# Kernel tuning notes

Hardware: AMD Instinct MI355X
Metric: run time of the kernel (lower is better)

Reference implementation:

```python
import jax, jax.numpy as jnp
import numpy as np

RADII = np.array([0.5, 1.0, 1.5, 2.0], dtype=np.float32)
SIGMA = 0.5          # gaussian radial-function width (= radius spacing)
EPS = 1e-8
N_SH = 9             # real spherical harmonics up to l=2
N_BASIS = len(RADII) * N_SH


def real_sh_l2(u):
    """Real spherical harmonics l=0,1,2 of unit vectors u[..., 3] -> [..., 9]."""
    x, y, z = u[..., 0], u[..., 1], u[..., 2]
    one = jnp.ones_like(x)
    return jnp.stack([
        0.28209479 * one,
        0.48860251 * x, 0.48860251 * y, 0.48860251 * z,
        1.09254843 * x * y,
        1.09254843 * y * z,
        0.31539157 * (3.0 * z * z - 1.0),
        1.09254843 * x * z,
        0.54627421 * (x * x - y * y),
    ], axis=-1)


def setup_inputs() -> dict:
    key = jax.random.key(0)
    k1, k2, k3, k4, k5 = jax.random.split(key, 5)
    n, c_in, d_out, b, a = 4, 32, 32, 8192, 32
    inp = jax.random.normal(k1, (n, c_in, b), jnp.float32)
    coords = jax.random.uniform(k2, (n, b, 3), jnp.float32) * 4.0
    neighbors = jax.random.randint(k3, (n, b, a), 0, b)
    relative_mask = jax.random.uniform(k4, (n, b, a), jnp.float32)
    W = jax.random.normal(k5, (d_out, c_in, N_BASIS), jnp.float32) / np.sqrt(c_in * N_BASIS)
    return {"input": inp, "coords": coords, "relative_mask": relative_mask,
            "W": W, "neighbors": neighbors}


def reference(input, coords, relative_mask, W, neighbors):
    n, c, b = input.shape
    idx_n = jnp.arange(n)[:, None, None]                     # [n,1,1]
    # neighbor difference matrix: coords[neighbors] - coords  -> [n,b,a,3]
    neigh_xyz = coords[idx_n, neighbors]
    diff = neigh_xyz - coords[:, :, None, :]
    r = jnp.linalg.norm(diff, axis=-1)                       # [n,b,a]
    u = diff / (r[..., None] + EPS)
    Y = real_sh_l2(u)                                        # [n,b,a,9]
    radii = jnp.asarray(RADII)
    rb = jnp.exp(-((r[..., None] - radii) / SIGMA) ** 2)     # [n,b,a,4]
    basis = (rb[..., :, None] * Y[..., None, :]).reshape(r.shape + (-1,))  # [n,b,a,36]
    # neighbor feature matrix: input[n, :, neighbors[n,b,a]] -> [n,b,a,c]
    feat = input[idx_n, :, neighbors]
    # relative_mask multiplies k over (n,b,a) == masking gathered features
    feat = feat * relative_mask[..., None]
    # fused form of: k[d,c,n,b,a] = sum_k basis[n,b,a,k] W[d,c,k];
    # out[n,d,b] = sum_{c,a} feat[n,b,a,c] * k[d,c,n,b,a]
    M = jnp.einsum('nbac,nbak->nbck', feat, basis)           # [n,b,c,36]
    return jnp.einsum('nbck,dck->ndb', M, W)
```

## Files before the change

### kernel.cpp

```cpp
#include <hip/hip_runtime.h>
#include <hip/hip_bf16.h>


typedef _Float16 f16x8 __attribute__((ext_vector_type(8)));
typedef _Float16 f16x4 __attribute__((ext_vector_type(4)));
typedef __fp16   h16x2 __attribute__((ext_vector_type(2)));
typedef float    f32x4 __attribute__((ext_vector_type(4)));
typedef unsigned int u32;

__device__ __forceinline__ u32 pk16(float a, float b) {
    union { h16x2 v; u32 u; } cv;
    cv.v = __builtin_amdgcn_cvt_pkrtz(a, b);
    return cv.u;
}
__device__ __forceinline__ unsigned short f16bits(float v) {
    const _Float16 hv = (_Float16)v;
    return __builtin_bit_cast(unsigned short, hv);
}

#define BAS_STRIDE 44

__device__ __forceinline__ void geom(float dx, float dy, float dz, float msk, int h_,
                                     float Y[9], float& rbA, float& rbB) {
    const float d2  = dx * dx + dy * dy + dz * dz;
    const float inv = rsqrtf(d2 + 1e-16f);
    const float r   = d2 * inv;
    const float x = dx * inv, y = dy * inv, z = dz * inv;
    Y[0] = 0.28209479f;
    Y[1] = 0.48860251f * x;
    Y[2] = 0.48860251f * y;
    Y[3] = 0.48860251f * z;
    Y[4] = 1.09254843f * x * y;
    Y[5] = 1.09254843f * y * z;
    Y[6] = 0.31539157f * (3.0f * z * z - 1.0f);
    Y[7] = 1.09254843f * x * z;
    Y[8] = 0.54627421f * (x * x - y * y);
    const float sA = r - (h_ ? 1.5f : 0.5f);
    const float sB = r - (h_ ? 2.0f : 1.0f);
    rbA = __expf(sA * sA * -4.0f) * msk;
    rbB = __expf(sB * sB * -4.0f) * msk;
}

__global__ __launch_bounds__(256) void prep_kernel(
    const float* __restrict__ inp, const float* __restrict__ W,
    const float* __restrict__ coords,
    unsigned short* __restrict__ inp_t16, unsigned short* __restrict__ Wfrag,
    float* __restrict__ coords4)
{
    if (blockIdx.x < 1024) {
        __shared__ float T[32][33];
        const int n  = blockIdx.x >> 8;
        const int b0 = (blockIdx.x & 255) << 5;
        const int bx = threadIdx.x & 31;
        const int cy = threadIdx.x >> 5;
        #pragma unroll
        for (int r = 0; r < 4; ++r) {
            const int cc = cy + r * 8;
            T[bx][cc] = inp[((n << 5) + cc) * 8192 + b0 + bx];
        }
        __syncthreads();
        const int cpos = ((bx & 15) << 1) | (bx >> 4);
        #pragma unroll
        for (int r = 0; r < 4; ++r) {
            const int by = cy + r * 8;
            inp_t16[((n << 13) + b0 + by) * 32 + cpos] = f16bits(T[by][bx]);
        }
    } else if (blockIdx.x < 1168) {
        const int t = (blockIdx.x - 1024) * 256 + threadIdx.x;
        if (t < 36 * 2 * 64 * 8) {
            const int j  = t & 7;
            const int l  = (t >> 3) & 63;
            const int dt = (t >> 9) & 1;
            const int kt = t >> 10;
            const int d  = dt * 16 + (l & 15);
            const int c  = ((l >> 4) << 3) + j;
            Wfrag[t] = f16bits(W[d * 1152 + c * 36 + kt]);
        }
    } else {
        const int t = (blockIdx.x - 1168) * 256 + threadIdx.x;
        f32x4 v;
        v[0] = coords[3 * t + 0];
        v[1] = coords[3 * t + 1];
        v[2] = coords[3 * t + 2];
        v[3] = 0.0f;
        *(f32x4*)(coords4 + ((size_t)t << 2)) = v;
    }
}

__global__ __launch_bounds__(512, 4) void se3_main(
    const unsigned short* __restrict__ inp_t16, const float* __restrict__ coords4,
    const float* __restrict__ rmask, const int* __restrict__ neigh,
    const unsigned short* __restrict__ Wfrag, float* __restrict__ out)
{
    __shared__ __align__(16) unsigned short Mb_s[36 * 580];
    __shared__ __align__(16) unsigned short bas[8][37 * BAS_STRIDE];
    __shared__ unsigned short idxs[16][32];
    __shared__ __align__(16) float Cp[8 * 64 * 4];

    const int tid  = threadIdx.x;
    const int lane = tid & 63;
    const int w    = tid >> 6;
    const int l15  = lane & 15;
    const int q    = lane >> 4;
    const int a_   = lane & 31;
    const int h_   = lane >> 5;

    const int blk = blockIdx.x;
    const int n_  = (blk & 7) >> 1;
    const int pos = ((blk >> 3) << 1) | (blk & 1);
    const int b0  = pos << 4;
    const int gp0 = (n_ << 13) | b0;
    const int nbase_pt = n_ << 13;
    const unsigned short* __restrict__ inp_n = inp_t16 + ((size_t)n_ << 18);

    unsigned short* basw = &bas[w][0];

    const int dt  = w >> 2;
    const int seg = w & 3;
    const int kt0 = seg * 9;
    f16x8 wf0, wf1, wf2, wf3, wf4, wf5, wf6, wf7, wf8;
    {
        const unsigned short* wb = &Wfrag[((size_t)((kt0 * 2 + dt) * 64 + lane)) << 3];
        wf0 = *(const f16x8*)(wb + 0 * 1024);
        wf1 = *(const f16x8*)(wb + 1 * 1024);
        wf2 = *(const f16x8*)(wb + 2 * 1024);
        wf3 = *(const f16x8*)(wb + 3 * 1024);
        wf4 = *(const f16x8*)(wb + 4 * 1024);
        wf5 = *(const f16x8*)(wb + 5 * 1024);
        wf6 = *(const f16x8*)(wb + 6 * 1024);
        wf7 = *(const f16x8*)(wb + 7 * 1024);
        wf8 = *(const f16x8*)(wb + 8 * 1024);
    }

    const int ph0 = 2 * l15;
    const int ph1 = (l15 < 2) ? (32 + 2 * l15) : (2 * l15 - 3);
    const int ph2 = (l15 < 4) ? (29 + 2 * l15) : 36;
    const int offB0 = ph0 * BAS_STRIDE + (q << 3);
    const int offB1 = ph1 * BAS_STRIDE + (q << 3);
    const int offB2 = ph2 * BAS_STRIDE + (q << 3);

    const int pA = w << 1, pB = pA | 1;
    const int gpA = gp0 + pA, gpB = gp0 + pB;

    const int   idxA = neigh[(gpA << 5) | a_];
    const int   idxB = neigh[(gpB << 5) | a_];
    const float mskA = rmask[(gpA << 5) | a_];
    const float mskB = rmask[(gpB << 5) | a_];
    const f32x4 cA4 = *(const f32x4*)(coords4 + ((size_t)gpA << 2));
    const f32x4 cB4 = *(const f32x4*)(coords4 + ((size_t)gpB << 2));
    if (lane < 32) {
        idxs[pA][a_] = (unsigned short)idxA;
        idxs[pB][a_] = (unsigned short)idxB;
    }
    const f32x4 nA4 = *(const f32x4*)(coords4 + ((size_t)(nbase_pt + idxA) << 2));
    const f32x4 nB4 = *(const f32x4*)(coords4 + ((size_t)(nbase_pt + idxB) << 2));
    const float dxA = nA4[0] - cA4[0], dyA = nA4[1] - cA4[1], dzA = nA4[2] - cA4[2];
    const float dxB = nB4[0] - cB4[0], dyB = nB4[1] - cB4[1], dzB = nB4[2] - cB4[2];

    u32 gA[8], gB[8];
    #pragma unroll
    for (int j = 0; j < 8; ++j) {
        const int ri = idxs[pA][(q << 3) + j];
        gA[j] = *(const u32*)(inp_n + (((unsigned)ri) << 5) + (l15 << 1));
    }
    #pragma unroll
    for (int j = 0; j < 8; ++j) {
        const int ri = idxs[pB][(q << 3) + j];
        gB[j] = *(const u32*)(inp_n + (((unsigned)ri) << 5) + (l15 << 1));
    }

    float YA[9], YB[9], rbA_A, rbB_A, rbA_B, rbB_B;
    geom(dxA, dyA, dzA, mskA, h_, YA, rbA_A, rbB_A);
    geom(dxB, dyB, dzB, mskB, h_, YB, rbA_B, rbB_B);

    #pragma unroll
    for (int t = 0; t < 18; ++t) {
        const float v = (t < 9) ? rbA_A * YA[t] : rbB_A * YA[t - 9];
        basw[(2 * t + h_) * BAS_STRIDE + a_] = f16bits(v);
    }

    f16x4 blo, bhi;
    blo = *(const f16x4*)&basw[offB0]; bhi = *(const f16x4*)&basw[offB0 + 4];
    const f16x8 BfA0 = __builtin_shufflevector(blo, bhi, 0, 1, 2, 3, 4, 5, 6, 7);
    blo = *(const f16x4*)&basw[offB1]; bhi = *(const f16x4*)&basw[offB1 + 4];
    const f16x8 BfA1 = __builtin_shufflevector(blo, bhi, 0, 1, 2, 3, 4, 5, 6, 7);
    blo = *(const f16x4*)&basw[offB2]; bhi = *(const f16x4*)&basw[offB2 + 4];
    const f16x8 BfA2 = __builtin_shufflevector(blo, bhi, 0, 1, 2, 3, 4, 5, 6, 7);

    union { f16x8 v; u32 u[4]; } afA0, afA1, afB0, afB1;
    #pragma unroll
    for (int j4 = 0; j4 < 4; ++j4) {
        afA0.u[j4] = __builtin_amdgcn_perm(gA[2 * j4 + 1], gA[2 * j4], 0x05040100u);
        afA1.u[j4] = __builtin_amdgcn_perm(gA[2 * j4 + 1], gA[2 * j4], 0x07060302u);
    }
    const f32x4 z4 = {0.0f, 0.0f, 0.0f, 0.0f};
    f32x4 DA00 = __builtin_amdgcn_mfma_f32_16x16x32_f16(afA0.v, BfA0, z4, 0, 0, 0);
    f32x4 DA01 = __builtin_amdgcn_mfma_f32_16x16x32_f16(afA0.v, BfA1, z4, 0, 0, 0);
    f32x4 DA02 = __builtin_amdgcn_mfma_f32_16x16x32_f16(afA0.v, BfA2, z4, 0, 0, 0);
    f32x4 DA10 = __builtin_amdgcn_mfma_f32_16x16x32_f16(afA1.v, BfA0, z4, 0, 0, 0);
    f32x4 DA11 = __builtin_amdgcn_mfma_f32_16x16x32_f16(afA1.v, BfA1, z4, 0, 0, 0);
    f32x4 DA12 = __builtin_amdgcn_mfma_f32_16x16x32_f16(afA1.v, BfA2, z4, 0, 0, 0);

    #pragma unroll
    for (int t = 0; t < 18; ++t) {
        const float v = (t < 9) ? rbA_B * YB[t] : rbB_B * YB[t - 9];
        basw[(2 * t + h_) * BAS_STRIDE + a_] = f16bits(v);
    }
    blo = *(const f16x4*)&basw[offB0]; bhi = *(const f16x4*)&basw[offB0 + 4];
    const f16x8 BfB0 = __builtin_shufflevector(blo, bhi, 0, 1, 2, 3, 4, 5, 6, 7);
    blo = *(const f16x4*)&basw[offB1]; bhi = *(const f16x4*)&basw[offB1 + 4];
    const f16x8 BfB1 = __builtin_shufflevector(blo, bhi, 0, 1, 2, 3, 4, 5, 6, 7);
    blo = *(const f16x4*)&basw[offB2]; bhi = *(const f16x4*)&basw[offB2 + 4];
    const f16x8 BfB2 = __builtin_shufflevector(blo, bhi, 0, 1, 2, 3, 4, 5, 6, 7);

    #pragma unroll
    for (int j4 = 0; j4 < 4; ++j4) {
        afB0.u[j4] = __builtin_amdgcn_perm(gB[2 * j4 + 1], gB[2 * j4], 0x05040100u);
        afB1.u[j4] = __builtin_amdgcn_perm(gB[2 * j4 + 1], gB[2 * j4], 0x07060302u);
    }
    f32x4 DB00 = __builtin_amdgcn_mfma_f32_16x16x32_f16(afB0.v, BfB0, z4, 0, 0, 0);
    f32x4 DB01 = __builtin_amdgcn_mfma_f32_16x16x32_f16(afB0.v, BfB1, z4, 0, 0, 0);
    f32x4 DB02 = __builtin_amdgcn_mfma_f32_16x16x32_f16(afB0.v, BfB2, z4, 0, 0, 0);
    f32x4 DB10 = __builtin_amdgcn_mfma_f32_16x16x32_f16(afB1.v, BfB0, z4, 0, 0, 0);
    f32x4 DB11 = __builtin_amdgcn_mfma_f32_16x16x32_f16(afB1.v, BfB1, z4, 0, 0, 0);
    f32x4 DB12 = __builtin_amdgcn_mfma_f32_16x16x32_f16(afB1.v, BfB2, z4, 0, 0, 0);

    {
        const int rowpA = pA * 36 + (q << 2);
        const int a0 = l15 * 580 + rowpA;
        const int a1 = (16 + l15) * 580 + rowpA;
        *(u32*)&Mb_s[a0]      = pk16(DA00[0], DA00[1]);
        *(u32*)&Mb_s[a0 + 2]  = pk16(DA00[2], DA00[3]);
        *(u32*)&Mb_s[a0 + 16] = pk16(DA10[0], DA10[1]);
        *(u32*)&Mb_s[a0 + 18] = pk16(DA10[2], DA10[3]);
        *(u32*)&Mb_s[a1]      = pk16(DA01[0], DA01[1]);
        *(u32*)&Mb_s[a1 + 2]  = pk16(DA01[2], DA01[3]);
        *(u32*)&Mb_s[a1 + 16] = pk16(DA11[0], DA11[1]);
        *(u32*)&Mb_s[a1 + 18] = pk16(DA11[2], DA11[3]);
        const int rowpB = pB * 36 + (q << 2);
        const int c0 = l15 * 580 + rowpB;
        const int c1 = (16 + l15) * 580 + rowpB;
        *(u32*)&Mb_s[c0]      = pk16(DB00[0], DB00[1]);
        *(u32*)&Mb_s[c0 + 2]  = pk16(DB00[2], DB00[3]);
        *(u32*)&Mb_s[c0 + 16] = pk16(DB10[0], DB10[1]);
        *(u32*)&Mb_s[c0 + 18] = pk16(DB10[2], DB10[3]);
        *(u32*)&Mb_s[c1]      = pk16(DB01[0], DB01[1]);
        *(u32*)&Mb_s[c1 + 2]  = pk16(DB01[2], DB01[3]);
        *(u32*)&Mb_s[c1 + 16] = pk16(DB11[0], DB11[1]);
        *(u32*)&Mb_s[c1 + 18] = pk16(DB11[2], DB11[3]);
        if (l15 < 4) {
            const int a2 = (32 + l15) * 580 + rowpA;
            *(u32*)&Mb_s[a2]      = pk16(DA02[0], DA02[1]);
            *(u32*)&Mb_s[a2 + 2]  = pk16(DA02[2], DA02[3]);
            *(u32*)&Mb_s[a2 + 16] = pk16(DA12[0], DA12[1]);
            *(u32*)&Mb_s[a2 + 18] = pk16(DA12[2], DA12[3]);
            const int c2 = (32 + l15) * 580 + rowpB;
            *(u32*)&Mb_s[c2]      = pk16(DB02[0], DB02[1]);
            *(u32*)&Mb_s[c2 + 2]  = pk16(DB02[2], DB02[3]);
            *(u32*)&Mb_s[c2 + 16] = pk16(DB12[0], DB12[1]);
            *(u32*)&Mb_s[c2 + 18] = pk16(DB12[2], DB12[3]);
        }
    }
    __syncthreads();

    {
        f32x4 acc2 = {0.0f, 0.0f, 0.0f, 0.0f};
        #define P2_STEP(I, WF)                                                       \
        {                                                                            \
            const int mbase = (kt0 + I) * 580 + l15 * 36 + (q << 3);                 \
            const f16x4 mlo = *(const f16x4*)&Mb_s[mbase];                           \
            const f16x4 mhi = *(const f16x4*)&Mb_s[mbase + 4];                       \
            const f16x8 bf  = __builtin_shufflevector(mlo, mhi, 0,1,2,3,4,5,6,7);    \
            acc2 = __builtin_amdgcn_mfma_f32_16x16x32_f16(WF, bf, acc2, 0, 0, 0);    \
        }
        P2_STEP(0, wf0) P2_STEP(1, wf1) P2_STEP(2, wf2)
        P2_STEP(3, wf3) P2_STEP(4, wf4) P2_STEP(5, wf5)
        P2_STEP(6, wf6) P2_STEP(7, wf7) P2_STEP(8, wf8)
        #undef P2_STEP
        *(f32x4*)&Cp[(w * 64 + lane) * 4] = acc2;
    }
    __syncthreads();

    if (w < 2) {
        const int dt2 = w;
        f32x4 s = *(const f32x4*)&Cp[((dt2 * 4 + 0) * 64 + lane) * 4];
        #pragma unroll
        for (int rphase = 1; rphase < 4; ++rphase) {
            const f32x4 t = *(const f32x4*)&Cp[((dt2 * 4 + rphase) * 64 + lane) * 4];
            s[0] += t[0]; s[1] += t[1]; s[2] += t[2]; s[3] += t[3];
        }
        const int drow = dt2 * 16 + (lane >> 4) * 4;
        const int col  = b0 + (lane & 15);
        #pragma unroll
        for (int rr = 0; rr < 4; ++rr) {
            out[(((n_ << 5) + drow + rr) << 13) + col] = s[rr];
        }
    }
}

extern "C" void kernel_launch(void* const* d_in, const int* in_sizes, int n_in,
                              void* d_out, int out_size, void* d_ws, size_t ws_size,
                              hipStream_t stream)
{
    const float* inp    = (const float*)d_in[0];
    const float* coords = (const float*)d_in[1];
    const float* rmask  = (const float*)d_in[2];
    const float* W      = (const float*)d_in[3];
    const int*   neigh  = (const int*)d_in[4];
    float*       outp   = (float*)d_out;

    unsigned short* inp_t16 = (unsigned short*)d_ws;
    unsigned short* Wfrag   = (unsigned short*)((char*)d_ws + (2u << 20));
    float*          coords4 = (float*)((char*)d_ws + (4u << 20));

    prep_kernel<<<1296, 256, 0, stream>>>(inp, W, coords, inp_t16, Wfrag, coords4);
    se3_main<<<2048, 512, 0, stream>>>(inp_t16, coords4, rmask, neigh, Wfrag, outp);
}
```

Before: 88.69 us.

## Make main kernel persistent over four tiles with prefetched neighbor gathers

Each block now handles four 16-point tiles in a loop, so the grid shrinks from 2048 to 512 blocks. The W fragment register loads are amortised across tiles. The next tile's indices, masks, coords and feature gathers are issued before the phase-2 MFMAs of the current tile so their latency overlaps compute. Neighbor indices are shared through ds_bpermute instead of a shared-memory index array, which removes that LDS buffer and its dependency. In exchange, register pressure from the double-buffered gathers goes up, and fewer blocks may leave CUs underfilled.

```diff
diff --git a/kernel.cpp b/kernel.cpp
--- a/kernel.cpp
+++ b/kernel.cpp
@@ -41,6 +41,21 @@
     rbB = __expf(sB * sB * -4.0f) * msk;
 }
 
+__device__ __forceinline__ void gather16(const unsigned short* __restrict__ inp_n,
+                                         int q, int l15, int idxA, int idxB,
+                                         u32* gA, u32* gB) {
+    #pragma unroll
+    for (int j = 0; j < 8; ++j) {
+        const int riA = __builtin_amdgcn_ds_bpermute((((q << 3) + j) << 2), idxA);
+        gA[j] = *(const u32*)(inp_n + (((unsigned)riA) << 5) + (l15 << 1));
+    }
+    #pragma unroll
+    for (int j = 0; j < 8; ++j) {
+        const int riB = __builtin_amdgcn_ds_bpermute((((q << 3) + j) << 2), idxB);
+        gB[j] = *(const u32*)(inp_n + (((unsigned)riB) << 5) + (l15 << 1));
+    }
+}
+
 __global__ __launch_bounds__(256) void prep_kernel(
     const float* __restrict__ inp, const float* __restrict__ W,
     const float* __restrict__ coords,
@@ -94,7 +109,6 @@
 {
     __shared__ __align__(16) unsigned short Mb_s[36 * 580];
     __shared__ __align__(16) unsigned short bas[8][37 * BAS_STRIDE];
-    __shared__ unsigned short idxs[16][32];
     __shared__ __align__(16) float Cp[8 * 64 * 4];
 
     const int tid  = threadIdx.x;
@@ -108,8 +122,6 @@
     const int blk = blockIdx.x;
     const int n_  = (blk & 7) >> 1;
     const int pos = ((blk >> 3) << 1) | (blk & 1);
-    const int b0  = pos << 4;
-    const int gp0 = (n_ << 13) | b0;
     const int nbase_pt = n_ << 13;
     const unsigned short* __restrict__ inp_n = inp_t16 + ((size_t)n_ << 18);
 
@@ -140,162 +152,180 @@
     const int offB2 = ph2 * BAS_STRIDE + (q << 3);
 
     const int pA = w << 1, pB = pA | 1;
-    const int gpA = gp0 + pA, gpB = gp0 + pB;
-
-    const int   idxA = neigh[(gpA << 5) | a_];
-    const int   idxB = neigh[(gpB << 5) | a_];
-    const float mskA = rmask[(gpA << 5) | a_];
-    const float mskB = rmask[(gpB << 5) | a_];
-    const f32x4 cA4 = *(const f32x4*)(coords4 + ((size_t)gpA << 2));
-    const f32x4 cB4 = *(const f32x4*)(coords4 + ((size_t)gpB << 2));
-    if (lane < 32) {
-        idxs[pA][a_] = (unsigned short)idxA;
-        idxs[pB][a_] = (unsigned short)idxB;
-    }
-    const f32x4 nA4 = *(const f32x4*)(coords4 + ((size_t)(nbase_pt + idxA) << 2));
-    const f32x4 nB4 = *(const f32x4*)(coords4 + ((size_t)(nbase_pt + idxB) << 2));
-    const float dxA = nA4[0] - cA4[0], dyA = nA4[1] - cA4[1], dzA = nA4[2] - cA4[2];
-    const float dxB = nB4[0] - cB4[0], dyB = nB4[1] - cB4[1], dzB = nB4[2] - cB4[2];
-
+
+#define LOADTILE(T, oidxA, oidxB, omskA, omskB, ocA, ocB, onA, onB) do {      \
+        const int _gpA = (n_ << 13) + (((pos << 2) | (T)) << 4) + pA;         \
+        const int _gpB = _gpA + 1;                                            \
+        oidxA = neigh[(_gpA << 5) | a_];                                      \
+        oidxB = neigh[(_gpB << 5) | a_];                                      \
+        omskA = rmask[(_gpA << 5) | a_];                                      \
+        omskB = rmask[(_gpB << 5) | a_];                                      \
+        ocA = *(const f32x4*)(coords4 + ((size_t)_gpA << 2));                 \
+        ocB = *(const f32x4*)(coords4 + ((size_t)_gpB << 2));                 \
+        onA = *(const f32x4*)(coords4 + ((size_t)(nbase_pt + oidxA) << 2));   \
+        onB = *(const f32x4*)(coords4 + ((size_t)(nbase_pt + oidxB) << 2));   \
+    } while (0)
+
+    int   idxA, idxB;
+    float mskA, mskB;
+    f32x4 cA4, cB4, nA4, nB4;
+    LOADTILE(0, idxA, idxB, mskA, mskB, cA4, cB4, nA4, nB4);
     u32 gA[8], gB[8];
+    gather16(inp_n, q, l15, idxA, idxB, gA, gB);
+
+    const f32x4 z4 = {0.0f, 0.0f, 0.0f, 0.0f};
+
     #pragma unroll
-    for (int j = 0; j < 8; ++j) {
-        const int ri = idxs[pA][(q << 3) + j];
-        gA[j] = *(const u32*)(inp_n + (((unsigned)ri) << 5) + (l15 << 1));
-    }
-    #pragma unroll
-    for (int j = 0; j < 8; ++j) {
-        const int ri = idxs[pB][(q << 3) + j];
-        gB[j] = *(const u32*)(inp_n + (((unsigned)ri) << 5) + (l15 << 1));
-    }
-
-    float YA[9], YB[9], rbA_A, rbB_A, rbA_B, rbB_B;
-    geom(dxA, dyA, dzA, mskA, h_, YA, rbA_A, rbB_A);
-    geom(dxB, dyB, dzB, mskB, h_, YB, rbA_B, rbB_B);
-
-    #pragma unroll
-    for (int t = 0; t < 18; ++t) {
-        const float v = (t < 9) ? rbA_A * YA[t] : rbB_A * YA[t - 9];
-        basw[(2 * t + h_) * BAS_STRIDE + a_] = f16bits(v);
-    }
-
-    f16x4 blo, bhi;
-    blo = *(const f16x4*)&basw[offB0]; bhi = *(const f16x4*)&basw[offB0 + 4];
-    const f16x8 BfA0 = __builtin_shufflevector(blo, bhi, 0, 1, 2, 3, 4, 5, 6, 7);
-    blo = *(const f16x4*)&basw[offB1]; bhi = *(const f16x4*)&basw[offB1 + 4];
-    const f16x8 BfA1 = __builtin_shufflevector(blo, bhi, 0, 1, 2, 3, 4, 5, 6, 7);
-    blo = *(const f16x4*)&basw[offB2]; bhi = *(const f16x4*)&basw[offB2 + 4];
-    const f16x8 BfA2 = __builtin_shufflevector(blo, bhi, 0, 1, 2, 3, 4, 5, 6, 7);
-
-    union { f16x8 v; u32 u[4]; } afA0, afA1, afB0, afB1;
-    #pragma unroll
-    for (int j4 = 0; j4 < 4; ++j4) {
-        afA0.u[j4] = __builtin_amdgcn_perm(gA[2 * j4 + 1], gA[2 * j4], 0x05040100u);
-        afA1.u[j4] = __builtin_amdgcn_perm(gA[2 * j4 + 1], gA[2 * j4], 0x07060302u);
-    }
-    const f32x4 z4 = {0.0f, 0.0f, 0.0f, 0.0f};
-    f32x4 DA00 = __builtin_amdgcn_mfma_f32_16x16x32_f16(afA0.v, BfA0, z4, 0, 0, 0);
-    f32x4 DA01 = __builtin_amdgcn_mfma_f32_16x16x32_f16(afA0.v, BfA1, z4, 0, 0, 0);
-    f32x4 DA02 = __builtin_amdgcn_mfma_f32_16x16x32_f16(afA0.v, BfA2, z4, 0, 0, 0);
-    f32x4 DA10 = __builtin_amdgcn_mfma_f32_16x16x32_f16(afA1.v, BfA0, z4, 0, 0, 0);
-    f32x4 DA11 = __builtin_amdgcn_mfma_f32_16x16x32_f16(afA1.v, BfA1, z4, 0, 0, 0);
-    f32x4 DA12 = __builtin_amdgcn_mfma_f32_16x16x32_f16(afA1.v, BfA2, z4, 0, 0, 0);
-
-    #pragma unroll
-    for (int t = 0; t < 18; ++t) {
-        const float v = (t < 9) ? rbA_B * YB[t] : rbB_B * YB[t - 9];
-        basw[(2 * t + h_) * BAS_STRIDE + a_] = f16bits(v);
-    }
-    blo = *(const f16x4*)&basw[offB0]; bhi = *(const f16x4*)&basw[offB0 + 4];
-    const f16x8 BfB0 = __builtin_shufflevector(blo, bhi, 0, 1, 2, 3, 4, 5, 6, 7);
-    blo = *(const f16x4*)&basw[offB1]; bhi = *(const f16x4*)&basw[offB1 + 4];
-    const f16x8 BfB1 = __builtin_shufflevector(blo, bhi, 0, 1, 2, 3, 4, 5, 6, 7);
-    blo = *(const f16x4*)&basw[offB2]; bhi = *(const f16x4*)&basw[offB2 + 4];
-    const f16x8 BfB2 = __builtin_shufflevector(blo, bhi, 0, 1, 2, 3, 4, 5, 6, 7);
-
-    #pragma unroll
-    for (int j4 = 0; j4 < 4; ++j4) {
-        afB0.u[j4] = __builtin_amdgcn_perm(gB[2 * j4 + 1], gB[2 * j4], 0x05040100u);
-        afB1.u[j4] = __builtin_amdgcn_perm(gB[2 * j4 + 1], gB[2 * j4], 0x07060302u);
-    }
-    f32x4 DB00 = __builtin_amdgcn_mfma_f32_16x16x32_f16(afB0.v, BfB0, z4, 0, 0, 0);
-    f32x4 DB01 = __builtin_amdgcn_mfma_f32_16x16x32_f16(afB0.v, BfB1, z4, 0, 0, 0);
-    f32x4 DB02 = __builtin_amdgcn_mfma_f32_16x16x32_f16(afB0.v, BfB2, z4, 0, 0, 0);
-    f32x4 DB10 = __builtin_amdgcn_mfma_f32_16x16x32_f16(afB1.v, BfB0, z4, 0, 0, 0);
-    f32x4 DB11 = __builtin_amdgcn_mfma_f32_16x16x32_f16(afB1.v, BfB1, z4, 0, 0, 0);
-    f32x4 DB12 = __builtin_amdgcn_mfma_f32_16x16x32_f16(afB1.v, BfB2, z4, 0, 0, 0);
-
-    {
-        const int rowpA = pA * 36 + (q << 2);
-        const int a0 = l15 * 580 + rowpA;
-        const int a1 = (16 + l15) * 580 + rowpA;
-        *(u32*)&Mb_s[a0]      = pk16(DA00[0], DA00[1]);
-        *(u32*)&Mb_s[a0 + 2]  = pk16(DA00[2], DA00[3]);
-        *(u32*)&Mb_s[a0 + 16] = pk16(DA10[0], DA10[1]);
-        *(u32*)&Mb_s[a0 + 18] = pk16(DA10[2], DA10[3]);
-        *(u32*)&Mb_s[a1]      = pk16(DA01[0], DA01[1]);
-        *(u32*)&Mb_s[a1 + 2]  = pk16(DA01[2], DA01[3]);
-        *(u32*)&Mb_s[a1 + 16] = pk16(DA11[0], DA11[1]);
-        *(u32*)&Mb_s[a1 + 18] = pk16(DA11[2], DA11[3]);
-        const int rowpB = pB * 36 + (q << 2);
-        const int c0 = l15 * 580 + rowpB;
-        const int c1 = (16 + l15) * 580 + rowpB;
-        *(u32*)&Mb_s[c0]      = pk16(DB00[0], DB00[1]);
-        *(u32*)&Mb_s[c0 + 2]  = pk16(DB00[2], DB00[3]);
-        *(u32*)&Mb_s[c0 + 16] = pk16(DB10[0], DB10[1]);
-        *(u32*)&Mb_s[c0 + 18] = pk16(DB10[2], DB10[3]);
-        *(u32*)&Mb_s[c1]      = pk16(DB01[0], DB01[1]);
-        *(u32*)&Mb_s[c1 + 2]  = pk16(DB01[2], DB01[3]);
-        *(u32*)&Mb_s[c1 + 16] = pk16(DB11[0], DB11[1]);
-        *(u32*)&Mb_s[c1 + 18] = pk16(DB11[2], DB11[3]);
-        if (l15 < 4) {
-            const int a2 = (32 + l15) * 580 + rowpA;
-            *(u32*)&Mb_s[a2]      = pk16(DA02[0], DA02[1]);
-            *(u32*)&Mb_s[a2 + 2]  = pk16(DA02[2], DA02[3]);
-            *(u32*)&Mb_s[a2 + 16] = pk16(DA12[0], DA12[1]);
-            *(u32*)&Mb_s[a2 + 18] = pk16(DA12[2], DA12[3]);
-            const int c2 = (32 + l15) * 580 + rowpB;
-            *(u32*)&Mb_s[c2]      = pk16(DB02[0], DB02[1]);
-            *(u32*)&Mb_s[c2 + 2]  = pk16(DB02[2], DB02[3]);
-            *(u32*)&Mb_s[c2 + 16] = pk16(DB12[0], DB12[1]);
-            *(u32*)&Mb_s[c2 + 18] = pk16(DB12[2], DB12[3]);
-        }
-    }
-    __syncthreads();
-
-    {
-        f32x4 acc2 = {0.0f, 0.0f, 0.0f, 0.0f};
-        #define P2_STEP(I, WF)                                                       \
-        {                                                                            \
-            const int mbase = (kt0 + I) * 580 + l15 * 36 + (q << 3);                 \
-            const f16x4 mlo = *(const f16x4*)&Mb_s[mbase];                           \
-            const f16x4 mhi = *(const f16x4*)&Mb_s[mbase + 4];                       \
-            const f16x8 bf  = __builtin_shufflevector(mlo, mhi, 0,1,2,3,4,5,6,7);    \
-            acc2 = __builtin_amdgcn_mfma_f32_16x16x32_f16(WF, bf, acc2, 0, 0, 0);    \
-        }
-        P2_STEP(0, wf0) P2_STEP(1, wf1) P2_STEP(2, wf2)
-        P2_STEP(3, wf3) P2_STEP(4, wf4) P2_STEP(5, wf5)
-        P2_STEP(6, wf6) P2_STEP(7, wf7) P2_STEP(8, wf8)
-        #undef P2_STEP
-        *(f32x4*)&Cp[(w * 64 + lane) * 4] = acc2;
-    }
-    __syncthreads();
-
-    if (w < 2) {
-        const int dt2 = w;
-        f32x4 s = *(const f32x4*)&Cp[((dt2 * 4 + 0) * 64 + lane) * 4];
-        #pragma unroll
-        for (int rphase = 1; rphase < 4; ++rphase) {
-            const f32x4 t = *(const f32x4*)&Cp[((dt2 * 4 + rphase) * 64 + lane) * 4];
-            s[0] += t[0]; s[1] += t[1]; s[2] += t[2]; s[3] += t[3];
-        }
-        const int drow = dt2 * 16 + (lane >> 4) * 4;
-        const int col  = b0 + (lane & 15);
-        #pragma unroll
-        for (int rr = 0; rr < 4; ++rr) {
-            out[(((n_ << 5) + drow + rr) << 13) + col] = s[rr];
-        }
-    }
+    for (int t = 0; t < 4; ++t) {
+        const int b0t = ((pos << 2) | t) << 4;
+
+        float YA[9], YB[9], rbA_A, rbB_A, rbA_B, rbB_B;
+        geom(nA4[0] - cA4[0], nA4[1] - cA4[1], nA4[2] - cA4[2], mskA, h_, YA, rbA_A, rbB_A);
+        geom(nB4[0] - cB4[0], nB4[1] - cB4[1], nB4[2] - cB4[2], mskB, h_, YB, rbA_B, rbB_B);
+
+        #pragma unroll
+        for (int tt = 0; tt < 18; ++tt) {
+            const float v = (tt < 9) ? rbA_A * YA[tt] : rbB_A * YA[tt - 9];
+            basw[(2 * tt + h_) * BAS_STRIDE + a_] = f16bits(v);
+        }
+
+        f16x4 blo, bhi;
+        blo = *(const f16x4*)&basw[offB0]; bhi = *(const f16x4*)&basw[offB0 + 4];
+        const f16x8 BfA0 = __builtin_shufflevector(blo, bhi, 0, 1, 2, 3, 4, 5, 6, 7);
+        blo = *(const f16x4*)&basw[offB1]; bhi = *(const f16x4*)&basw[offB1 + 4];
+        const f16x8 BfA1 = __builtin_shufflevector(blo, bhi, 0, 1, 2, 3, 4, 5, 6, 7);
+        blo = *(const f16x4*)&basw[offB2]; bhi = *(const f16x4*)&basw[offB2 + 4];
+        const f16x8 BfA2 = __builtin_shufflevector(blo, bhi, 0, 1, 2, 3, 4, 5, 6, 7);
+
+        union { f16x8 v; u32 u[4]; } afA0, afA1, afB0, afB1;
+        #pragma unroll
+        for (int j4 = 0; j4 < 4; ++j4) {
+            afA0.u[j4] = __builtin_amdgcn_perm(gA[2 * j4 + 1], gA[2 * j4], 0x05040100u);
+            afA1.u[j4] = __builtin_amdgcn_perm(gA[2 * j4 + 1], gA[2 * j4], 0x07060302u);
+        }
+        f32x4 DA00 = __builtin_amdgcn_mfma_f32_16x16x32_f16(afA0.v, BfA0, z4, 0, 0, 0);
+        f32x4 DA01 = __builtin_amdgcn_mfma_f32_16x16x32_f16(afA0.v, BfA1, z4, 0, 0, 0);
+        f32x4 DA02 = __builtin_amdgcn_mfma_f32_16x16x32_f16(afA0.v, BfA2, z4, 0, 0, 0);
+        f32x4 DA10 = __builtin_amdgcn_mfma_f32_16x16x32_f16(afA1.v, BfA0, z4, 0, 0, 0);
+        f32x4 DA11 = __builtin_amdgcn_mfma_f32_16x16x32_f16(afA1.v, BfA1, z4, 0, 0, 0);
+        f32x4 DA12 = __builtin_amdgcn_mfma_f32_16x16x32_f16(afA1.v, BfA2, z4, 0, 0, 0);
+
+        #pragma unroll
+        for (int tt = 0; tt < 18; ++tt) {
+            const float v = (tt < 9) ? rbA_B * YB[tt] : rbB_B * YB[tt - 9];
+            basw[(2 * tt + h_) * BAS_STRIDE + a_] = f16bits(v);
+        }
+        blo = *(const f16x4*)&basw[offB0]; bhi = *(const f16x4*)&basw[offB0 + 4];
+        const f16x8 BfB0 = __builtin_shufflevector(blo, bhi, 0, 1, 2, 3, 4, 5, 6, 7);
+        blo = *(const f16x4*)&basw[offB1]; bhi = *(const f16x4*)&basw[offB1 + 4];
+        const f16x8 BfB1 = __builtin_shufflevector(blo, bhi, 0, 1, 2, 3, 4, 5, 6, 7);
+        blo = *(const f16x4*)&basw[offB2]; bhi = *(const f16x4*)&basw[offB2 + 4];
+        const f16x8 BfB2 = __builtin_shufflevector(blo, bhi, 0, 1, 2, 3, 4, 5, 6, 7);
+
+        #pragma unroll
+        for (int j4 = 0; j4 < 4; ++j4) {
+            afB0.u[j4] = __builtin_amdgcn_perm(gB[2 * j4 + 1], gB[2 * j4], 0x05040100u);
+            afB1.u[j4] = __builtin_amdgcn_perm(gB[2 * j4 + 1], gB[2 * j4], 0x07060302u);
+        }
+        f32x4 DB00 = __builtin_amdgcn_mfma_f32_16x16x32_f16(afB0.v, BfB0, z4, 0, 0, 0);
+        f32x4 DB01 = __builtin_amdgcn_mfma_f32_16x16x32_f16(afB0.v, BfB1, z4, 0, 0, 0);
+        f32x4 DB02 = __builtin_amdgcn_mfma_f32_16x16x32_f16(afB0.v, BfB2, z4, 0, 0, 0);
+        f32x4 DB10 = __builtin_amdgcn_mfma_f32_16x16x32_f16(afB1.v, BfB0, z4, 0, 0, 0);
+        f32x4 DB11 = __builtin_amdgcn_mfma_f32_16x16x32_f16(afB1.v, BfB1, z4, 0, 0, 0);
+        f32x4 DB12 = __builtin_amdgcn_mfma_f32_16x16x32_f16(afB1.v, BfB2, z4, 0, 0, 0);
+
+        int   nidxA = 0, nidxB = 0;
+        float nmskA = 0.f, nmskB = 0.f;
+        f32x4 ncA4 = z4, ncB4 = z4, nnA4 = z4, nnB4 = z4;
+        if (t < 3) {
+            LOADTILE(t + 1, nidxA, nidxB, nmskA, nmskB, ncA4, ncB4, nnA4, nnB4);
+        }
+
+        {
+            const int rowpA = pA * 36 + (q << 2);
+            const int a0 = l15 * 580 + rowpA;
+            const int a1 = (16 + l15) * 580 + rowpA;
+            *(u32*)&Mb_s[a0]      = pk16(DA00[0], DA00[1]);
+            *(u32*)&Mb_s[a0 + 2]  = pk16(DA00[2], DA00[3]);
+            *(u32*)&Mb_s[a0 + 16] = pk16(DA10[0], DA10[1]);
+            *(u32*)&Mb_s[a0 + 18] = pk16(DA10[2], DA10[3]);
+            *(u32*)&Mb_s[a1]      = pk16(DA01[0], DA01[1]);
+            *(u32*)&Mb_s[a1 + 2]  = pk16(DA01[2], DA01[3]);
+            *(u32*)&Mb_s[a1 + 16] = pk16(DA11[0], DA11[1]);
+            *(u32*)&Mb_s[a1 + 18] = pk16(DA11[2], DA11[3]);
+            const int rowpB = pB * 36 + (q << 2);
+            const int c0 = l15 * 580 + rowpB;
+            const int c1 = (16 + l15) * 580 + rowpB;
+            *(u32*)&Mb_s[c0]      = pk16(DB00[0], DB00[1]);
+            *(u32*)&Mb_s[c0 + 2]  = pk16(DB00[2], DB00[3]);
+            *(u32*)&Mb_s[c0 + 16] = pk16(DB10[0], DB10[1]);
+            *(u32*)&Mb_s[c0 + 18] = pk16(DB10[2], DB10[3]);
+            *(u32*)&Mb_s[c1]      = pk16(DB01[0], DB01[1]);
+            *(u32*)&Mb_s[c1 + 2]  = pk16(DB01[2], DB01[3]);
+            *(u32*)&Mb_s[c1 + 16] = pk16(DB11[0], DB11[1]);
+            *(u32*)&Mb_s[c1 + 18] = pk16(DB11[2], DB11[3]);
+            if (l15 < 4) {
+                const int a2 = (32 + l15) * 580 + rowpA;
+                *(u32*)&Mb_s[a2]      = pk16(DA02[0], DA02[1]);
+                *(u32*)&Mb_s[a2 + 2]  = pk16(DA02[2], DA02[3]);
+                *(u32*)&Mb_s[a2 + 16] = pk16(DA12[0], DA12[1]);
+                *(u32*)&Mb_s[a2 + 18] = pk16(DA12[2], DA12[3]);
+                const int c2 = (32 + l15) * 580 + rowpB;
+                *(u32*)&Mb_s[c2]      = pk16(DB02[0], DB02[1]);
+                *(u32*)&Mb_s[c2 + 2]  = pk16(DB02[2], DB02[3]);
+                *(u32*)&Mb_s[c2 + 16] = pk16(DB12[0], DB12[1]);
+                *(u32*)&Mb_s[c2 + 18] = pk16(DB12[2], DB12[3]);
+            }
+        }
+        __syncthreads();
+
+        u32 ngA[8], ngB[8];
+        if (t < 3) {
+            gather16(inp_n, q, l15, nidxA, nidxB, ngA, ngB);
+        }
+
+        {
+            f32x4 acc2 = {0.0f, 0.0f, 0.0f, 0.0f};
+            #define P2_STEP(I, WF)                                                       \
+            {                                                                            \
+                const int mbase = (kt0 + I) * 580 + l15 * 36 + (q << 3);                 \
+                const f16x4 mlo = *(const f16x4*)&Mb_s[mbase];                           \
+                const f16x4 mhi = *(const f16x4*)&Mb_s[mbase + 4];                       \
+                const f16x8 bf  = __builtin_shufflevector(mlo, mhi, 0,1,2,3,4,5,6,7);    \
+                acc2 = __builtin_amdgcn_mfma_f32_16x16x32_f16(WF, bf, acc2, 0, 0, 0);    \
+            }
+            P2_STEP(0, wf0) P2_STEP(1, wf1) P2_STEP(2, wf2)
+            P2_STEP(3, wf3) P2_STEP(4, wf4) P2_STEP(5, wf5)
+            P2_STEP(6, wf6) P2_STEP(7, wf7) P2_STEP(8, wf8)
+            #undef P2_STEP
+            *(f32x4*)&Cp[(w * 64 + lane) * 4] = acc2;
+        }
+        __syncthreads();
+
+        if (w < 2) {
+            const int dt2 = w;
+            f32x4 s = *(const f32x4*)&Cp[((dt2 * 4 + 0) * 64 + lane) * 4];
+            #pragma unroll
+            for (int rphase = 1; rphase < 4; ++rphase) {
+                const f32x4 tt = *(const f32x4*)&Cp[((dt2 * 4 + rphase) * 64 + lane) * 4];
+                s[0] += tt[0]; s[1] += tt[1]; s[2] += tt[2]; s[3] += tt[3];
+            }
+            const int drow = dt2 * 16 + (lane >> 4) * 4;
+            const int col  = b0t + (lane & 15);
+            #pragma unroll
+            for (int rr = 0; rr < 4; ++rr) {
+                out[(((n_ << 5) + drow + rr) << 13) + col] = s[rr];
+            }
+        }
+
+        if (t < 3) {
+            idxA = nidxA; idxB = nidxB; mskA = nmskA; mskB = nmskB;
+            cA4 = ncA4; cB4 = ncB4; nA4 = nnA4; nB4 = nnB4;
+            #pragma unroll
+            for (int j = 0; j < 8; ++j) { gA[j] = ngA[j]; gB[j] = ngB[j]; }
+        }
+    }
+#undef LOADTILE
 }
 
 extern "C" void kernel_launch(void* const* d_in, const int* in_sizes, int n_in,
@@ -314,5 +344,5 @@
     float*          coords4 = (float*)((char*)d_ws + (4u << 20));
 
     prep_kernel<<<1296, 256, 0, stream>>>(inp, W, coords, inp_t16, Wfrag, coords4);
-    se3_main<<<2048, 512, 0, stream>>>(inp_t16, coords4, rmask, neigh, Wfrag, outp);
-}
+    se3_main<<<512, 512, 0, stream>>>(inp_t16, coords4, rmask, neigh, Wfrag, outp);
+}
```

New measurement: 92.95 us. 4.8% more time.
